# Performance work log

Hardware: AMD Instinct MI355X
Metric: run time of the kernel (lower is better)

Reference implementation:

```python
import jax, jax.numpy as jnp
import numpy as np

N_NODES = 50000
N_EDGES = 800000
IN_CH = 256
HID = 32
HEADS = 8
OUT_CH = 64
NEG_SLOPE = 0.2


def _glorot(key, shape):
    fan = shape[0] + shape[-1]
    lim = jnp.sqrt(6.0 / fan)
    return jax.random.uniform(key, shape, jnp.float32, -lim, lim)


def setup_inputs() -> dict:
    key = jax.random.key(0)
    ks = jax.random.split(key, 12)
    x = jax.random.normal(ks[0], (N_NODES, IN_CH), jnp.float32)
    edge_index = jax.random.randint(ks[1], (2, N_EDGES), 0, N_NODES, jnp.int64 if jax.config.jax_enable_x64 else jnp.int32)
    # conv1: in -> heads*hid, concat
    W1 = _glorot(ks[2], (IN_CH, HEADS * HID))
    a_src1 = _glorot(ks[3], (HEADS, HID))
    a_dst1 = _glorot(ks[4], (HEADS, HID))
    b1 = jnp.zeros((HEADS * HID,), jnp.float32)
    # conv2: heads*hid -> heads*hid, 1 head
    W2 = _glorot(ks[5], (HEADS * HID, HEADS * HID))
    a_src2 = _glorot(ks[6], (1, HEADS * HID))
    a_dst2 = _glorot(ks[7], (1, HEADS * HID))
    b2 = jnp.zeros((HEADS * HID,), jnp.float32)
    # final linear
    Wlin = _glorot(ks[8], (HEADS * HID, OUT_CH))
    blin = jnp.zeros((OUT_CH,), jnp.float32)
    return {"x": x, "edge_index": edge_index, "W1": W1, "a_src1": a_src1,
            "a_dst1": a_dst1, "b1": b1, "W2": W2, "a_src2": a_src2,
            "a_dst2": a_dst2, "b2": b2, "Wlin": Wlin, "blin": blin}


def gat_conv(x, src, dst, W, a_src, a_dst, bias, heads, out_ch):
    n = x.shape[0]
    h = (x @ W).reshape(n, heads, out_ch)            # [N, H, C]
    # per-node attention halves, then gather per edge (cheaper than edge-first)
    s = jnp.einsum('nhc,hc->nh', h, a_src)[src]      # [E, H]
    d = jnp.einsum('nhc,hc->nh', h, a_dst)[dst]      # [E, H]
    e = jax.nn.leaky_relu(s + d, NEG_SLOPE)          # [E, H]
    # segment softmax over incoming edges of each dst node
    emax = jax.ops.segment_max(e, dst, num_segments=n)
    e = jnp.exp(e - jax.lax.stop_gradient(emax)[dst])
    denom = jax.ops.segment_sum(e, dst, num_segments=n)
    alpha = e / denom[dst]                           # [E, H]
    msg = h[src] * alpha[:, :, None]                 # [E, H, C]
    out = jax.ops.segment_sum(msg, dst, num_segments=n)
    return out.reshape(n, heads * out_ch) + bias


def reference(x, edge_index, W1, a_src1, a_dst1, b1, W2, a_src2, a_dst2, b2, Wlin, blin):
    n = x.shape[0]
    # PyG GATConv adds self-loops by default
    loops = jnp.arange(n, dtype=edge_index.dtype)
    src = jnp.concatenate([edge_index[0], loops])
    dst = jnp.concatenate([edge_index[1], loops])
    # dropout (p=0.6) is identity in eval mode
    h = jax.nn.elu(gat_conv(x, src, dst, W1, a_src1, a_dst1, b1, HEADS, HID))
    h = jax.nn.elu(gat_conv(h, src, dst, W2, a_src2, a_dst2, b2, 1, HEADS * HID))
    return h @ Wlin + blin
```

## Files before the change

### kernel.cpp

```cpp
#include <hip/hip_runtime.h>
#include <hip/hip_bf16.h>
#include <hip/hip_fp16.h>

typedef __attribute__((ext_vector_type(8))) short short8;
typedef __attribute__((ext_vector_type(4))) float f32x4;

#define GLL(g, s) __builtin_amdgcn_global_load_lds(                        \
    (const __attribute__((address_space(1))) void*)(g),                    \
    (__attribute__((address_space(3))) void*)(s), 16, 0, 0)

__device__ __forceinline__ ushort f2bf(float f) {
    unsigned u = __float_as_uint(f);
    u += 0x7fffu + ((u >> 16) & 1u);
    return (ushort)(u >> 16);
}
__device__ __forceinline__ float bf2f(ushort h) {
    return __uint_as_float(((unsigned)h) << 16);
}
__device__ __forceinline__ float elu_f(float x) {
    return x > 0.0f ? x : expm1f(x);
}
__device__ __forceinline__ float lrelu(float x) {
    return x < 0.0f ? 0.2f * x : x;
}

__global__ void hist_kernel(const int* __restrict__ ei, int* __restrict__ deg, int E, int n) {
    int total = E + n;
    for (int i = blockIdx.x * blockDim.x + threadIdx.x; i < total; i += gridDim.x * blockDim.x) {
        int d = (i < E) ? ei[E + i] : (i - E);
        atomicAdd(&deg[d], 1);
    }
}

__global__ __launch_bounds__(256) void partial_kernel(const int* __restrict__ deg, int* __restrict__ bsums, int n) {
    __shared__ int sm[256];
    int t = threadIdx.x;
    int idx = blockIdx.x * 256 + t;
    sm[t] = (idx < n) ? deg[idx] : 0;
    __syncthreads();
    #pragma unroll
    for (int off = 128; off > 0; off >>= 1) {
        if (t < off) sm[t] += sm[t + off];
        __syncthreads();
    }
    if (t == 0) bsums[blockIdx.x] = sm[0];
}

__global__ __launch_bounds__(256) void scanblocks_kernel(const int* __restrict__ bsums, int* __restrict__ boff,
                                                         int* __restrict__ rowptr, int nb, int n) {
    __shared__ int sm[256];
    int t = threadIdx.x;
    int carry = 0;
    for (int base = 0; base < nb; base += 256) {
        int i = base + t;
        int v = (i < nb) ? bsums[i] : 0;
        sm[t] = v;
        __syncthreads();
        #pragma unroll
        for (int off = 1; off < 256; off <<= 1) {
            int x = (t >= off) ? sm[t - off] : 0;
            __syncthreads();
            sm[t] += x;
            __syncthreads();
        }
        if (i < nb) boff[i] = carry + sm[t] - v;
        int tot = sm[255];
        __syncthreads();
        carry += tot;
    }
    if (t == 0) rowptr[n] = carry;
}

__global__ __launch_bounds__(256) void finalize_kernel(const int* __restrict__ deg, const int* __restrict__ boff,
                                                       int* __restrict__ rowptr, int* __restrict__ cursor, int n) {
    __shared__ int sm[256];
    int t = threadIdx.x;
    int idx = blockIdx.x * 256 + t;
    int v = (idx < n) ? deg[idx] : 0;
    sm[t] = v;
    __syncthreads();
    #pragma unroll
    for (int off = 1; off < 256; off <<= 1) {
        int x = (t >= off) ? sm[t - off] : 0;
        __syncthreads();
        sm[t] += x;
        __syncthreads();
    }
    if (idx < n) {
        int ex = boff[blockIdx.x] + sm[t] - v;
        rowptr[idx] = ex;
        cursor[idx] = ex;
    }
}

__global__ void scatter_kernel(const int* __restrict__ ei, int* __restrict__ cursor,
                               int* __restrict__ csr_src, int E, int n) {
    int total = E + n;
    for (int i = blockIdx.x * blockDim.x + threadIdx.x; i < total; i += gridDim.x * blockDim.x) {
        int s, d;
        if (i < E) { s = ei[i]; d = ei[E + i]; }
        else       { s = i - E; d = s; }
        int pos = atomicAdd(&cursor[d], 1);
        csr_src[pos] = s;
    }
}

__global__ void wconv_kernel(const float* __restrict__ W, short* __restrict__ hi,
                             short* __restrict__ lo, int KN, int Ncols) {
    int idx = blockIdx.x * 256 + threadIdx.x;
    if (idx >= KN) return;
    int k = idx / Ncols, n = idx - k * Ncols;
    float v = W[idx];
    ushort h = f2bf(v);
    ushort l = f2bf(v - bf2f(h));
    size_t o = ((size_t)(k >> 3) * Ncols + n) * 8 + (k & 7);
    hi[o] = (short)h;
    lo[o] = (short)l;
}

template<int N, bool OUTHALF>
__global__ __launch_bounds__(256, 2) void gemm_mfma(const float* __restrict__ A,
                                                    const short* __restrict__ Bph,
                                                    const short* __restrict__ Bpl,
                                                    const float* __restrict__ bias,
                                                    void* __restrict__ Cout, int M) {
    constexpr int FN = (N == 256) ? 4 : 1;
    __shared__ short Bh[2][N * 32], Bl[2][N * 32];
    const int tid = threadIdx.x;
    const int lane = tid & 63;
    const int wave = tid >> 6;
    const int r0 = blockIdx.x * 64;
    const int c = lane >> 4;
    const int rs = lane & 15;
    const int wn0 = wave * (N / 4);

    const float* aBase[4];
    #pragma unroll
    for (int fm = 0; fm < 4; ++fm) {
        int r = r0 + fm * 16 + rs;
        if (r > M - 1) r = M - 1;
        aBase[fm] = A + (size_t)r * 256 + c * 8;
    }

    auto issueB = [&](int buf, int t) {
        if constexpr (N == 256) {
            #pragma unroll
            for (int q = 0; q < 4; ++q) {
                const short* sh = Bph + ((size_t)(t * 4 + q) * 256 + tid) * 8;
                const short* sl = Bpl + ((size_t)(t * 4 + q) * 256 + tid) * 8;
                short* dh = &Bh[buf][q * 2048 + wave * 512];
                short* dl = &Bl[buf][q * 2048 + wave * 512];
                GLL(sh, dh);
                GLL(sl, dl);
            }
        } else {
            const short* sh = Bph + ((size_t)(t * 4 + wave) * 64 + lane) * 8;
            const short* sl = Bpl + ((size_t)(t * 4 + wave) * 64 + lane) * 8;
            short* dh = &Bh[buf][wave * 512];
            short* dl = &Bl[buf][wave * 512];
            GLL(sh, dh);
            GLL(sl, dl);
        }
    };

    float4 aregA[8], aregB[8];
    auto loadA = [&](float4* ar, int t) {
        #pragma unroll
        for (int fm = 0; fm < 4; ++fm) {
            ar[2 * fm]     = *(const float4*)(aBase[fm] + t * 32);
            ar[2 * fm + 1] = *(const float4*)(aBase[fm] + t * 32 + 4);
        }
    };
    auto convA = [&](const float4* ar, short8* ah, short8* al) {
        #pragma unroll
        for (int fm = 0; fm < 4; ++fm) {
            float f[8] = {ar[2 * fm].x, ar[2 * fm].y, ar[2 * fm].z, ar[2 * fm].w,
                          ar[2 * fm + 1].x, ar[2 * fm + 1].y, ar[2 * fm + 1].z, ar[2 * fm + 1].w};
            short8 hi, lo;
            #pragma unroll
            for (int j = 0; j < 8; ++j) {
                ushort hb = f2bf(f[j]);
                hi[j] = (short)hb;
                lo[j] = (short)f2bf(f[j] - bf2f(hb));
            }
            ah[fm] = hi;
            al[fm] = lo;
        }
    };

    f32x4 acc[4][FN];
    #pragma unroll
    for (int i = 0; i < 4; ++i)
        #pragma unroll
        for (int j = 0; j < FN; ++j)
            acc[i][j] = (f32x4){0.f, 0.f, 0.f, 0.f};

    loadA(aregA, 0);
    issueB(0, 0);
    __syncthreads();

    #pragma unroll
    for (int t = 0; t < 8; ++t) {
        float4* curA = (t & 1) ? aregB : aregA;
        float4* nxtA = (t & 1) ? aregA : aregB;
        if (t < 7) {
            loadA(nxtA, t + 1);
            issueB((t + 1) & 1, t + 1);
        }
        short8 ah[4], al[4];
        convA(curA, ah, al);
        #pragma unroll
        for (int fn = 0; fn < FN; ++fn) {
            int n = wn0 + fn * 16 + rs;
            int idx = c * N * 8 + n * 8;
            short8 bhv = *(const short8*)&Bh[t & 1][idx];
            short8 blv = *(const short8*)&Bl[t & 1][idx];
            #pragma unroll
            for (int fm = 0; fm < 4; ++fm) {
                acc[fm][fn] = __builtin_amdgcn_mfma_f32_16x16x32_bf16(ah[fm], bhv, acc[fm][fn], 0, 0, 0);
                acc[fm][fn] = __builtin_amdgcn_mfma_f32_16x16x32_bf16(ah[fm], blv, acc[fm][fn], 0, 0, 0);
                acc[fm][fn] = __builtin_amdgcn_mfma_f32_16x16x32_bf16(al[fm], bhv, acc[fm][fn], 0, 0, 0);
            }
        }
        __syncthreads();
    }

    #pragma unroll
    for (int fn = 0; fn < FN; ++fn) {
        int col = wn0 + fn * 16 + rs;
        float bv = bias ? bias[col] : 0.0f;
        #pragma unroll
        for (int fm = 0; fm < 4; ++fm) {
            #pragma unroll
            for (int g = 0; g < 4; ++g) {
                int r = r0 + fm * 16 + c * 4 + g;
                if (r < M) {
                    float v = acc[fm][fn][g] + bv;
                    if constexpr (OUTHALF)
                        ((__half*)Cout)[(size_t)r * N + col] = __float2half_rn(v);
                    else
                        ((float*)Cout)[(size_t)r * N + col] = v;
                }
            }
        }
    }
}

template<int HEADS>
__global__ __launch_bounds__(256) void sd_kernel(const __half* __restrict__ h, const float* __restrict__ a_src,
                                                 const float* __restrict__ a_dst, float* __restrict__ s_out,
                                                 float* __restrict__ d_out_, int nnodes) {
    int lane = threadIdx.x & 63;
    int node = blockIdx.x * 4 + (threadIdx.x >> 6);
    if (node >= nnodes) return;
    const __half2* hp = (const __half2*)(h + (size_t)node * 256 + lane * 4);
    float2 f01 = __half22float2(hp[0]);
    float2 f23 = __half22float2(hp[1]);
    float4 as = *(const float4*)&a_src[lane * 4];
    float4 ad = *(const float4*)&a_dst[lane * 4];
    float ps = f01.x * as.x + f01.y * as.y + f23.x * as.z + f23.y * as.w;
    float pd = f01.x * ad.x + f01.y * ad.y + f23.x * ad.z + f23.y * ad.w;
    const int GS = 64 / HEADS;
    #pragma unroll
    for (int off = 1; off < GS; off <<= 1) {
        ps += __shfl_xor(ps, off);
        pd += __shfl_xor(pd, off);
    }
    int g = lane / GS;
    int r = lane & (GS - 1);
    if (r == 0) s_out[(size_t)node * HEADS + g] = ps;
    if (r == 1) d_out_[(size_t)node * HEADS + g] = pd;
}

template<int HEADS>
__global__ __launch_bounds__(256) void agg_kernel(const int* __restrict__ rowptr, const int* __restrict__ csr_src,
                                                  const __half* __restrict__ h, const float* __restrict__ s_att,
                                                  const float* __restrict__ d_att, const float* __restrict__ bias,
                                                  float* __restrict__ out, int nnodes) {
    int lane = threadIdx.x & 63;
    int node = blockIdx.x * 4 + (threadIdx.x >> 6);
    if (node >= nnodes) return;
    const int hh = (HEADS == 8) ? (lane >> 3) : 0;
    const int cbase = lane * 4;
    const int begin = rowptr[node], end = rowptr[node + 1];
    const float dl = d_att[(size_t)node * HEADS + hh];
    float m = -1e30f, den = 0.f;
    float ax = 0.f, ay = 0.f, az = 0.f, aw = 0.f;
    int i = begin;
    for (; i + 4 <= end; i += 4) {
        int s0 = csr_src[i], s1 = csr_src[i + 1], s2 = csr_src[i + 2], s3 = csr_src[i + 3];
        const __half2* p0 = (const __half2*)(h + (size_t)s0 * 256 + cbase);
        const __half2* p1 = (const __half2*)(h + (size_t)s1 * 256 + cbase);
        const __half2* p2 = (const __half2*)(h + (size_t)s2 * 256 + cbase);
        const __half2* p3 = (const __half2*)(h + (size_t)s3 * 256 + cbase);
        __half2 q0a = p0[0], q0b = p0[1];
        __half2 q1a = p1[0], q1b = p1[1];
        __half2 q2a = p2[0], q2b = p2[1];
        __half2 q3a = p3[0], q3b = p3[1];
        float v0 = lrelu(s_att[(size_t)s0 * HEADS + hh] + dl);
        float v1 = lrelu(s_att[(size_t)s1 * HEADS + hh] + dl);
        float v2 = lrelu(s_att[(size_t)s2 * HEADS + hh] + dl);
        float v3 = lrelu(s_att[(size_t)s3 * HEADS + hh] + dl);
        float vb = fmaxf(fmaxf(v0, v1), fmaxf(v2, v3));
        float mn = fmaxf(m, vb);
        float sc = __expf(m - mn);
        float w0 = __expf(v0 - mn), w1 = __expf(v1 - mn);
        float w2 = __expf(v2 - mn), w3 = __expf(v3 - mn);
        m = mn;
        den = den * sc + (w0 + w1) + (w2 + w3);
        float2 f0a = __half22float2(q0a), f0b = __half22float2(q0b);
        float2 f1a = __half22float2(q1a), f1b = __half22float2(q1b);
        float2 f2a = __half22float2(q2a), f2b = __half22float2(q2b);
        float2 f3a = __half22float2(q3a), f3b = __half22float2(q3b);
        ax = ax * sc + w0 * f0a.x + w1 * f1a.x + w2 * f2a.x + w3 * f3a.x;
        ay = ay * sc + w0 * f0a.y + w1 * f1a.y + w2 * f2a.y + w3 * f3a.y;
        az = az * sc + w0 * f0b.x + w1 * f1b.x + w2 * f2b.x + w3 * f3b.x;
        aw = aw * sc + w0 * f0b.y + w1 * f1b.y + w2 * f2b.y + w3 * f3b.y;
    }
    for (; i < end; ++i) {
        int s0 = csr_src[i];
        const __half2* p0 = (const __half2*)(h + (size_t)s0 * 256 + cbase);
        __half2 q0a = p0[0], q0b = p0[1];
        float v0 = lrelu(s_att[(size_t)s0 * HEADS + hh] + dl);
        float mn = fmaxf(m, v0);
        float sc = __expf(m - mn);
        float w0 = __expf(v0 - mn);
        m = mn;
        den = den * sc + w0;
        float2 f0a = __half22float2(q0a), f0b = __half22float2(q0b);
        ax = ax * sc + w0 * f0a.x;
        ay = ay * sc + w0 * f0a.y;
        az = az * sc + w0 * f0b.x;
        aw = aw * sc + w0 * f0b.y;
    }
    float inv = 1.0f / den;
    float4 bv = *(const float4*)&bias[cbase];
    float4 r;
    r.x = elu_f(ax * inv + bv.x);
    r.y = elu_f(ay * inv + bv.y);
    r.z = elu_f(az * inv + bv.z);
    r.w = elu_f(aw * inv + bv.w);
    *(float4*)&out[(size_t)node * 256 + cbase] = r;
}

extern "C" void kernel_launch(void* const* d_in, const int* in_sizes, int n_in,
                              void* d_out, int out_size, void* d_ws, size_t ws_size,
                              hipStream_t stream) {
    const float* x      = (const float*)d_in[0];
    const int*   ei     = (const int*)d_in[1];
    const float* W1     = (const float*)d_in[2];
    const float* a_src1 = (const float*)d_in[3];
    const float* a_dst1 = (const float*)d_in[4];
    const float* b1     = (const float*)d_in[5];
    const float* W2     = (const float*)d_in[6];
    const float* a_src2 = (const float*)d_in[7];
    const float* a_dst2 = (const float*)d_in[8];
    const float* b2     = (const float*)d_in[9];
    const float* Wlin   = (const float*)d_in[10];
    const float* blin   = (const float*)d_in[11];
    float* out = (float*)d_out;

    const int N = in_sizes[0] / 256;
    const int E = in_sizes[1] / 2;
    const int ET = E + N;
    const int NB = (N + 255) / 256;

    char* p = (char*)d_ws;
    auto alloc = [&](size_t bytes) {
        void* r = (void*)p;
        p += (bytes + 255) & ~size_t(255);
        return r;
    };
    __half* bufH  = (__half*)alloc((size_t)N * 256 * 2);
    float* bufB   = (float*)alloc((size_t)N * 256 * 4);
    float* s1     = (float*)alloc((size_t)N * 8 * 4);
    float* d1     = (float*)alloc((size_t)N * 8 * 4);
    float* s2     = (float*)alloc((size_t)N * 4);
    float* d2     = (float*)alloc((size_t)N * 4);
    int*   deg    = (int*)alloc((size_t)N * 4);
    int*   cursor = (int*)alloc((size_t)N * 4);
    int*   rowptr = (int*)alloc((size_t)(N + 1) * 4);
    int*   csr    = (int*)alloc((size_t)ET * 4);
    int*   bsums  = (int*)alloc((size_t)NB * 4);
    int*   boff   = (int*)alloc((size_t)NB * 4);
    short* W1h    = (short*)alloc((size_t)256 * 256 * 2);
    short* W1l    = (short*)alloc((size_t)256 * 256 * 2);
    short* W2h    = (short*)alloc((size_t)256 * 256 * 2);
    short* W2l    = (short*)alloc((size_t)256 * 256 * 2);
    short* W3h    = (short*)alloc((size_t)256 * 64 * 2);
    short* W3l    = (short*)alloc((size_t)256 * 64 * 2);

    hipMemsetAsync(deg, 0, (size_t)N * 4, stream);
    hist_kernel<<<(ET + 255) / 256, 256, 0, stream>>>(ei, deg, E, N);
    partial_kernel<<<NB, 256, 0, stream>>>(deg, bsums, N);
    scanblocks_kernel<<<1, 256, 0, stream>>>(bsums, boff, rowptr, NB, N);
    finalize_kernel<<<NB, 256, 0, stream>>>(deg, boff, rowptr, cursor, N);
    scatter_kernel<<<(ET + 255) / 256, 256, 0, stream>>>(ei, cursor, csr, E, N);

    wconv_kernel<<<(256 * 256 + 255) / 256, 256, 0, stream>>>(W1, W1h, W1l, 256 * 256, 256);
    wconv_kernel<<<(256 * 256 + 255) / 256, 256, 0, stream>>>(W2, W2h, W2l, 256 * 256, 256);
    wconv_kernel<<<(256 * 64 + 255) / 256, 256, 0, stream>>>(Wlin, W3h, W3l, 256 * 64, 64);

    const int gBlocks = (N + 63) / 64;
    const int nodeBlocks = (N + 3) / 4;

    gemm_mfma<256, true><<<gBlocks, 256, 0, stream>>>(x, W1h, W1l, nullptr, bufH, N);
    sd_kernel<8><<<nodeBlocks, 256, 0, stream>>>(bufH, a_src1, a_dst1, s1, d1, N);
    agg_kernel<8><<<nodeBlocks, 256, 0, stream>>>(rowptr, csr, bufH, s1, d1, b1, bufB, N);

    gemm_mfma<256, true><<<gBlocks, 256, 0, stream>>>(bufB, W2h, W2l, nullptr, bufH, N);
    sd_kernel<1><<<nodeBlocks, 256, 0, stream>>>(bufH, a_src2, a_dst2, s2, d2, N);
    agg_kernel<1><<<nodeBlocks, 256, 0, stream>>>(rowptr, csr, bufH, s2, d2, b2, bufB, N);

    gemm_mfma<64, false><<<gBlocks, 256, 0, stream>>>(bufB, W3h, W3l, blin, out, N);
}
```

Before: 518.8 us.

## Give each wave private B staging and deepen GEMM prefetch without block barriers

The GEMM kernel now stages B tiles in per-wave shared-memory slices, so each wave loads only the columns it consumes. This lets the kernel drop the block-wide __syncthreads in favour of explicit vmcnt/lgkmcnt waits, with loads issued two k-steps ahead. The aim is to remove barrier stalls and hide more global-load latency, at the cost of duplicated B loads for the N<256 case and reliance on hand-counted waitcnt values. Separately, the aggregation kernel fetches each gathered half4 row chunk with one 8-byte load instead of two 4-byte loads.

```diff
diff --git a/kernel.cpp b/kernel.cpp
--- a/kernel.cpp
+++ b/kernel.cpp
@@ -125,14 +125,16 @@
                                                     const float* __restrict__ bias,
                                                     void* __restrict__ Cout, int M) {
     constexpr int FN = (N == 256) ? 4 : 1;
-    __shared__ short Bh[2][N * 32], Bl[2][N * 32];
+    __shared__ short Bh[4][2][4][64][8];
+    __shared__ short Bl[4][2][4][64][8];
     const int tid = threadIdx.x;
     const int lane = tid & 63;
     const int wave = tid >> 6;
     const int r0 = blockIdx.x * 64;
     const int c = lane >> 4;
     const int rs = lane & 15;
-    const int wn0 = wave * (N / 4);
+    const int c0 = (N == 256) ? wave * 64 : 0;
+    const int colin = (N == 256) ? rs : (wave * 16 + rs);
 
     const float* aBase[4];
     #pragma unroll
@@ -142,33 +144,21 @@
         aBase[fm] = A + (size_t)r * 256 + c * 8;
     }
 
-    auto issueB = [&](int buf, int t) {
-        if constexpr (N == 256) {
-            #pragma unroll
-            for (int q = 0; q < 4; ++q) {
-                const short* sh = Bph + ((size_t)(t * 4 + q) * 256 + tid) * 8;
-                const short* sl = Bpl + ((size_t)(t * 4 + q) * 256 + tid) * 8;
-                short* dh = &Bh[buf][q * 2048 + wave * 512];
-                short* dl = &Bl[buf][q * 2048 + wave * 512];
-                GLL(sh, dh);
-                GLL(sl, dl);
-            }
-        } else {
-            const short* sh = Bph + ((size_t)(t * 4 + wave) * 64 + lane) * 8;
-            const short* sl = Bpl + ((size_t)(t * 4 + wave) * 64 + lane) * 8;
-            short* dh = &Bh[buf][wave * 512];
-            short* dl = &Bl[buf][wave * 512];
-            GLL(sh, dh);
-            GLL(sl, dl);
-        }
-    };
-
     float4 aregA[8], aregB[8];
     auto loadA = [&](float4* ar, int t) {
         #pragma unroll
         for (int fm = 0; fm < 4; ++fm) {
             ar[2 * fm]     = *(const float4*)(aBase[fm] + t * 32);
             ar[2 * fm + 1] = *(const float4*)(aBase[fm] + t * 32 + 4);
+        }
+    };
+    auto issueB = [&](int buf, int t) {
+        #pragma unroll
+        for (int q = 0; q < 4; ++q) {
+            const short* sh = Bph + ((size_t)(t * 4 + q) * N + c0 + lane) * 8;
+            const short* sl = Bpl + ((size_t)(t * 4 + q) * N + c0 + lane) * 8;
+            GLL(sh, &Bh[wave][buf][q][0][0]);
+            GLL(sl, &Bl[wave][buf][q][0][0]);
         }
     };
     auto convA = [&](const float4* ar, short8* ah, short8* al) {
@@ -195,26 +185,21 @@
         for (int j = 0; j < FN; ++j)
             acc[i][j] = (f32x4){0.f, 0.f, 0.f, 0.f};
 
-    loadA(aregA, 0);
-    issueB(0, 0);
-    __syncthreads();
+    loadA(aregA, 0); issueB(0, 0);
+    loadA(aregB, 1); issueB(1, 1);
 
     #pragma unroll
     for (int t = 0; t < 8; ++t) {
-        float4* curA = (t & 1) ? aregB : aregA;
-        float4* nxtA = (t & 1) ? aregA : aregB;
-        if (t < 7) {
-            loadA(nxtA, t + 1);
-            issueB((t + 1) & 1, t + 1);
-        }
+        if (t < 7) asm volatile("s_waitcnt vmcnt(16)" ::: "memory");
+        else       asm volatile("s_waitcnt vmcnt(0)" ::: "memory");
+        const int cur = t & 1;
+        const float4* curA = (t & 1) ? aregB : aregA;
         short8 ah[4], al[4];
         convA(curA, ah, al);
         #pragma unroll
         for (int fn = 0; fn < FN; ++fn) {
-            int n = wn0 + fn * 16 + rs;
-            int idx = c * N * 8 + n * 8;
-            short8 bhv = *(const short8*)&Bh[t & 1][idx];
-            short8 blv = *(const short8*)&Bl[t & 1][idx];
+            short8 bhv = *(const short8*)&Bh[wave][cur][c][colin + fn * 16][0];
+            short8 blv = *(const short8*)&Bl[wave][cur][c][colin + fn * 16][0];
             #pragma unroll
             for (int fm = 0; fm < 4; ++fm) {
                 acc[fm][fn] = __builtin_amdgcn_mfma_f32_16x16x32_bf16(ah[fm], bhv, acc[fm][fn], 0, 0, 0);
@@ -222,9 +207,15 @@
                 acc[fm][fn] = __builtin_amdgcn_mfma_f32_16x16x32_bf16(al[fm], bhv, acc[fm][fn], 0, 0, 0);
             }
         }
-        __syncthreads();
-    }
-
+        asm volatile("s_waitcnt lgkmcnt(0)" ::: "memory");
+        if (t < 6) {
+            float4* nxtA = (t & 1) ? aregB : aregA;
+            loadA(nxtA, t + 2);
+            issueB(cur, t + 2);
+        }
+    }
+
+    const int wn0 = wave * (N / 4);
     #pragma unroll
     for (int fn = 0; fn < FN; ++fn) {
         int col = wn0 + fn * 16 + rs;
@@ -289,14 +280,10 @@
     int i = begin;
     for (; i + 4 <= end; i += 4) {
         int s0 = csr_src[i], s1 = csr_src[i + 1], s2 = csr_src[i + 2], s3 = csr_src[i + 3];
-        const __half2* p0 = (const __half2*)(h + (size_t)s0 * 256 + cbase);
-        const __half2* p1 = (const __half2*)(h + (size_t)s1 * 256 + cbase);
-        const __half2* p2 = (const __half2*)(h + (size_t)s2 * 256 + cbase);
-        const __half2* p3 = (const __half2*)(h + (size_t)s3 * 256 + cbase);
-        __half2 q0a = p0[0], q0b = p0[1];
-        __half2 q1a = p1[0], q1b = p1[1];
-        __half2 q2a = p2[0], q2b = p2[1];
-        __half2 q3a = p3[0], q3b = p3[1];
+        uint2 u0 = *(const uint2*)(h + (size_t)s0 * 256 + cbase);
+        uint2 u1 = *(const uint2*)(h + (size_t)s1 * 256 + cbase);
+        uint2 u2 = *(const uint2*)(h + (size_t)s2 * 256 + cbase);
+        uint2 u3 = *(const uint2*)(h + (size_t)s3 * 256 + cbase);
         float v0 = lrelu(s_att[(size_t)s0 * HEADS + hh] + dl);
         float v1 = lrelu(s_att[(size_t)s1 * HEADS + hh] + dl);
         float v2 = lrelu(s_att[(size_t)s2 * HEADS + hh] + dl);
@@ -308,10 +295,10 @@
         float w2 = __expf(v2 - mn), w3 = __expf(v3 - mn);
         m = mn;
         den = den * sc + (w0 + w1) + (w2 + w3);
-        float2 f0a = __half22float2(q0a), f0b = __half22float2(q0b);
-        float2 f1a = __half22float2(q1a), f1b = __half22float2(q1b);
-        float2 f2a = __half22float2(q2a), f2b = __half22float2(q2b);
-        float2 f3a = __half22float2(q3a), f3b = __half22float2(q3b);
+        float2 f0a = __half22float2(*(const __half2*)&u0.x), f0b = __half22float2(*(const __half2*)&u0.y);
+        float2 f1a = __half22float2(*(const __half2*)&u1.x), f1b = __half22float2(*(const __half2*)&u1.y);
+        float2 f2a = __half22float2(*(const __half2*)&u2.x), f2b = __half22float2(*(const __half2*)&u2.y);
+        float2 f3a = __half22float2(*(const __half2*)&u3.x), f3b = __half22float2(*(const __half2*)&u3.y);
         ax = ax * sc + w0 * f0a.x + w1 * f1a.x + w2 * f2a.x + w3 * f3a.x;
         ay = ay * sc + w0 * f0a.y + w1 * f1a.y + w2 * f2a.y + w3 * f3a.y;
         az = az * sc + w0 * f0b.x + w1 * f1b.x + w2 * f2b.x + w3 * f3b.x;
@@ -319,15 +306,14 @@
     }
     for (; i < end; ++i) {
         int s0 = csr_src[i];
-        const __half2* p0 = (const __half2*)(h + (size_t)s0 * 256 + cbase);
-        __half2 q0a = p0[0], q0b = p0[1];
+        uint2 u0 = *(const uint2*)(h + (size_t)s0 * 256 + cbase);
         float v0 = lrelu(s_att[(size_t)s0 * HEADS + hh] + dl);
         float mn = fmaxf(m, v0);
         float sc = __expf(m - mn);
         float w0 = __expf(v0 - mn);
         m = mn;
         den = den * sc + w0;
-        float2 f0a = __half22float2(q0a), f0b = __half22float2(q0b);
+        float2 f0a = __half22float2(*(const __half2*)&u0.x), f0b = __half22float2(*(const __half2*)&u0.y);
         ax = ax * sc + w0 * f0a.x;
         ay = ay * sc + w0 * f0a.y;
         az = az * sc + w0 * f0b.x;
```

Measured after the change: 517.4 us. About the same (-0.3%).
